# Optimization experiments

Hardware: AMD Instinct MI355X
Metric: run time of the kernel (lower is better)

## Reference

```python
import jax, jax.numpy as jnp
import numpy as np

B, T, C, H = 2, 2048, 1024, 16
D = C // H  # head_dim = 64

def setup_inputs() -> dict:
    key = jax.random.key(0)
    ks = jax.random.split(key, 5)
    x = jax.random.normal(ks[0], (B, T, C), dtype=jnp.float32)
    Wqkv = jax.random.normal(ks[1], (C, 3 * C), dtype=jnp.float32) * 0.02
    bqkv = jnp.zeros((3 * C,), dtype=jnp.float32)
    Wout = jax.random.normal(ks[2], (C, C), dtype=jnp.float32) * 0.02
    bout = jnp.zeros((C,), dtype=jnp.float32)
    return {"x": x, "Wqkv": Wqkv, "bqkv": bqkv, "Wout": Wout, "bout": bout}

def reference(x, Wqkv, bqkv, Wout, bout):
    Bb, Tt, Cc = x.shape
    qkv = x @ Wqkv + bqkv                       # [B,T,3C]
    qkv = qkv.reshape(Bb, Tt, 3, H, D)
    qkv = jnp.transpose(qkv, (2, 0, 3, 1, 4))   # [3,B,H,T,D]
    q, k, v = qkv[0], qkv[1], qkv[2]
    scale = 1.0 / np.sqrt(D).astype(np.float32)
    scores = jnp.einsum('bhqd,bhkd->bhqk', q, k) * scale  # [B,H,T,T]
    causal = jnp.tril(jnp.ones((Tt, Tt), dtype=bool))
    scores = jnp.where(causal[None, None, :, :], scores, jnp.float32(-jnp.inf))
    attn = jax.nn.softmax(scores, axis=-1)
    out = jnp.einsum('bhqk,bhkd->bhqd', attn, v)          # [B,H,T,D]
    out = jnp.transpose(out, (0, 2, 1, 3)).reshape(Bb, Tt, Cc)
    return out @ Wout + bout
```

## Files before the change

### kernel.cpp

```cpp
#include <hip/hip_runtime.h>

#define Bc 2
#define Tc 2048
#define Cc 1024
#define Hc 16
#define Dc 64
#define Mtot (Bc*Tc)
#define Kdim Cc
#define N1 (3*Cc)
#define N2 Cc

typedef __attribute__((ext_vector_type(8))) short short8;
typedef __attribute__((ext_vector_type(4))) float float4v;

__device__ __forceinline__ unsigned short f2bf(float f) {
  unsigned int u = __builtin_bit_cast(unsigned int, f);
  u += 0x7FFFu + ((u >> 16) & 1u);
  return (unsigned short)(u >> 16);
}

__device__ __forceinline__ unsigned int pk_bf16(float a, float b) {
#if __has_builtin(__builtin_amdgcn_cvt_pk_bf16_f32)
  typedef __attribute__((ext_vector_type(2))) __bf16 bf16x2;
  bf16x2 v = __builtin_amdgcn_cvt_pk_bf16_f32(a, b);
  return __builtin_bit_cast(unsigned int, v);
#else
  return (unsigned int)f2bf(a) | ((unsigned int)f2bf(b) << 16);
#endif
}

__device__ __forceinline__ void gl2lds16(const unsigned short* g, unsigned short* l) {
  __builtin_amdgcn_global_load_lds((const __attribute__((address_space(1))) void*)g,
                                   (__attribute__((address_space(3))) void*)l, 16, 0, 0);
}

__global__ __launch_bounds__(256) void k_prep(const float* __restrict__ wqkv,
                                              const float* __restrict__ wout,
                                              const float* __restrict__ x,
                                              unsigned short* __restrict__ wqkvT,
                                              unsigned short* __restrict__ woutT,
                                              unsigned short* __restrict__ xb) {
  const int bx = blockIdx.x;
  if (bx >= 128) {
    int idx = ((bx - 128) * 32 + blockIdx.y) * 256 + threadIdx.x;
    float4 v = ((const float4*)x)[idx];
    uint2 o;
    o.x = pk_bf16(v.x, v.y);
    o.y = pk_bf16(v.z, v.w);
    ((uint2*)xb)[idx] = o;
    return;
  }
  __shared__ float tile[32][33];
  const float* w;  unsigned short* wT;  int N, n0;
  if (bx < 96) { w = wqkv; wT = wqkvT; N = N1; n0 = bx * 32; }
  else         { w = wout; wT = woutT; N = N2; n0 = (bx - 96) * 32; }
  const int k0 = blockIdx.y * 32;
  int tx = threadIdx.x & 31, ty = threadIdx.x >> 5;
  for (int i = 0; i < 4; ++i)
    tile[ty + 8*i][tx] = w[(size_t)(k0 + ty + 8*i) * N + n0 + tx];
  __syncthreads();
  for (int i = 0; i < 4; ++i)
    wT[(size_t)(n0 + ty + 8*i) * Kdim + k0 + tx] = f2bf(tile[tx][ty + 8*i]);
}

__global__ __launch_bounds__(256) void k_gemm_qkv(const unsigned short* __restrict__ A,
                                                  const unsigned short* __restrict__ BT,
                                                  const float* __restrict__ bias,
                                                  unsigned short* __restrict__ qkv) {
  __shared__ alignas(16) unsigned short smem[64*136 + 64];
  unsigned short* As = smem;
  unsigned short* Bs = smem + 4096;
  const int m0 = blockIdx.y * 128, n0 = blockIdx.x * 128;
  const int tid = threadIdx.x;
  const int w = tid >> 6, lane = tid & 63;
  const int ln = lane & 15, qd = lane >> 4;
  const int wm = w >> 1, wn = w & 1;
  const int c0 = tid, c1 = tid + 256;
  const int row0 = c0 >> 2, ko0 = (c0 & 3) * 8;
  const int row1 = c1 >> 2, ko1 = (c1 & 3) * 8;
  const float4v zero4 = {0.f, 0.f, 0.f, 0.f};
  float4v acc[4][4];
  for (int i = 0; i < 4; ++i) for (int j = 0; j < 4; ++j) acc[i][j] = zero4;
  for (int kk = 0; kk < Kdim; kk += 32) {
    __syncthreads();
    gl2lds16(A  + (size_t)(m0 + row0) * Kdim + kk + ko0, As + c0 * 8);
    gl2lds16(A  + (size_t)(m0 + row1) * Kdim + kk + ko1, As + c1 * 8);
    gl2lds16(BT + (size_t)(n0 + row0) * Kdim + kk + ko0, Bs + c0 * 8);
    gl2lds16(BT + (size_t)(n0 + row1) * Kdim + kk + ko1, Bs + c1 * 8);
    __syncthreads();
    short8 af[4], bf[4];
    for (int i = 0; i < 4; ++i)
      af[i] = *(const short8*)(As + (wm*64 + i*16 + ln) * 32 + qd*8);
    for (int j = 0; j < 4; ++j)
      bf[j] = *(const short8*)(Bs + (wn*64 + j*16 + ln) * 32 + qd*8);
    for (int i = 0; i < 4; ++i)
      for (int j = 0; j < 4; ++j)
        acc[i][j] = __builtin_amdgcn_mfma_f32_16x16x32_bf16(af[i], bf[j], acc[i][j], 0, 0, 0);
  }
  const int s = n0 >> 10;
  if (s < 2) {
    const float scale = (s == 0) ? 0.125f : 1.0f;
    for (int i = 0; i < 4; ++i) {
      int mbase = m0 + wm*64 + i*16 + qd*4;
      for (int j = 0; j < 4; ++j) {
        int ncol = n0 + wn*64 + j*16 + ln;
        float bv = bias[ncol];
        int rem = ncol & 1023;
        int h = rem >> 6, d = rem & 63;
        for (int r = 0; r < 4; ++r) {
          int m = mbase + r;
          int b = m >> 11, t = m & 2047;
          float val = (acc[i][j][r] + bv) * scale;
          qkv[((((size_t)s*Bc + b)*Hc + h)*Tc + t)*Dc + d] = f2bf(val);
        }
      }
    }
  } else {
    unsigned short* vbase = qkv + (size_t)2*Bc*Hc*Tc*Dc;
    const int b = m0 >> 11, t0 = m0 & 2047;
    const int h0 = (n0 & 1023) >> 6;
    for (int p = 0; p < 2; ++p) {
      __syncthreads();
      if (wn == p) {
        for (int i = 0; i < 4; ++i) {
          int tl = wm*64 + i*16 + qd*4;
          for (int j = 0; j < 4; ++j) {
            int dl = j*16 + ln;
            float bv = bias[n0 + p*64 + dl];
            uint2 pk;
            pk.x = pk_bf16(acc[i][j][0] + bv, acc[i][j][1] + bv);
            pk.y = pk_bf16(acc[i][j][2] + bv, acc[i][j][3] + bv);
            *(uint2*)(smem + dl*136 + tl) = pk;
          }
        }
      }
      __syncthreads();
      for (int ii = 0; ii < 4; ++ii) {
        int idx = tid + 256*ii;
        int row = idx >> 4, c16 = idx & 15;
        int4 v = *(const int4*)(smem + row*136 + c16*8);
        *(int4*)(vbase + (((size_t)b*Hc + h0 + p)*Dc + row)*Tc + t0 + c16*8) = v;
      }
    }
  }
}

__global__ __launch_bounds__(256) void k_gemm_out(const unsigned short* __restrict__ A,
                                                  const unsigned short* __restrict__ BT,
                                                  const float* __restrict__ bias,
                                                  float* __restrict__ out) {
  __shared__ alignas(16) unsigned short As[64*32];
  __shared__ alignas(16) unsigned short Bs[128*32];
  const int m0 = blockIdx.y * 64, n0 = blockIdx.x * 128;
  const int tid = threadIdx.x;
  const int w = tid >> 6, lane = tid & 63;
  const int ln = lane & 15, qd = lane >> 4;
  const int wm = w >> 1, wn = w & 1;
  const int arow = tid >> 2, ako = (tid & 3) * 8;
  const int c0 = tid, c1 = tid + 256;
  const int brow0 = c0 >> 2, bko0 = (c0 & 3) * 8;
  const int brow1 = c1 >> 2, bko1 = (c1 & 3) * 8;
  const float4v zero4 = {0.f, 0.f, 0.f, 0.f};
  float4v acc[2][4];
  for (int i = 0; i < 2; ++i) for (int j = 0; j < 4; ++j) acc[i][j] = zero4;
  for (int kk = 0; kk < Kdim; kk += 32) {
    __syncthreads();
    gl2lds16(A  + (size_t)(m0 + arow)  * Kdim + kk + ako,  As + tid * 8);
    gl2lds16(BT + (size_t)(n0 + brow0) * Kdim + kk + bko0, Bs + c0 * 8);
    gl2lds16(BT + (size_t)(n0 + brow1) * Kdim + kk + bko1, Bs + c1 * 8);
    __syncthreads();
    short8 af[2], bf[4];
    for (int i = 0; i < 2; ++i)
      af[i] = *(const short8*)(As + (wm*32 + i*16 + ln) * 32 + qd*8);
    for (int j = 0; j < 4; ++j)
      bf[j] = *(const short8*)(Bs + (wn*64 + j*16 + ln) * 32 + qd*8);
    for (int i = 0; i < 2; ++i)
      for (int j = 0; j < 4; ++j)
        acc[i][j] = __builtin_amdgcn_mfma_f32_16x16x32_bf16(af[i], bf[j], acc[i][j], 0, 0, 0);
  }
  for (int i = 0; i < 2; ++i) {
    int mbase = m0 + wm*32 + i*16 + qd*4;
    for (int j = 0; j < 4; ++j) {
      int ncol = n0 + wn*64 + j*16 + ln;
      float bv = bias[ncol];
      for (int r = 0; r < 4; ++r)
        out[(size_t)(mbase + r) * N2 + ncol] = acc[i][j][r] + bv;
    }
  }
}

__device__ __forceinline__ void attn_substep(
    const unsigned short* __restrict__ Ks, const unsigned short* __restrict__ Vt,
    unsigned short* __restrict__ pw,
    const short8 qa0, const short8 qa1,
    float4v* o, float& m_i, float& l_i,
    int k0, int myq, bool mask, int ln, int qd)
{
  const float L2E = 1.44269504f;
  const float4v zero4 = {0.f, 0.f, 0.f, 0.f};
  float4v s[4];
  for (int ki = 0; ki < 4; ++ki) {
    s[ki] = zero4;
    const unsigned short* kr = Ks + (ki*16 + ln)*72;
    short8 kf0 = *(const short8*)(kr + qd*8);
    short8 kf1 = *(const short8*)(kr + 32 + qd*8);
    s[ki] = __builtin_amdgcn_mfma_f32_16x16x32_bf16(kf0, qa0, s[ki], 0, 0, 0);
    s[ki] = __builtin_amdgcn_mfma_f32_16x16x32_bf16(kf1, qa1, s[ki], 0, 0, 0);
  }
  if (mask) {
    for (int ki = 0; ki < 4; ++ki) {
      int key = k0 + ki*16 + qd*4;
      for (int r = 0; r < 4; ++r)
        if (key + r > myq) s[ki][r] = -1e30f;
    }
  }
  float mt = -1e30f;
  for (int ki = 0; ki < 4; ++ki)
    for (int r = 0; r < 4; ++r) mt = fmaxf(mt, s[ki][r]);
  mt = fmaxf(mt, __shfl_xor(mt, 16));
  mt = fmaxf(mt, __shfl_xor(mt, 32));
  float mn = fmaxf(m_i, mt);
  float al = exp2f((m_i - mn) * L2E);
  m_i = mn;
  float st = 0.f;
  for (int ki = 0; ki < 4; ++ki)
    for (int r = 0; r < 4; ++r) {
      s[ki][r] = exp2f((s[ki][r] - mn) * L2E);
      st += s[ki][r];
    }
  st += __shfl_xor(st, 16);
  st += __shfl_xor(st, 32);
  l_i = l_i * al + st;
  for (int dt = 0; dt < 4; ++dt)
    for (int r = 0; r < 4; ++r) o[dt][r] *= al;
  for (int ki = 0; ki < 4; ++ki) {
    uint2 p2;
    p2.x = pk_bf16(s[ki][0], s[ki][1]);
    p2.y = pk_bf16(s[ki][2], s[ki][3]);
    *(uint2*)(pw + ln*72 + ki*16 + qd*4) = p2;
  }
  short8 pb0 = *(const short8*)(pw + ln*72 + qd*8);
  short8 pb1 = *(const short8*)(pw + ln*72 + 32 + qd*8);
  for (int dt = 0; dt < 4; ++dt) {
    const unsigned short* vr = Vt + (dt*16 + ln)*72;
    short8 va0 = *(const short8*)(vr + qd*8);
    short8 va1 = *(const short8*)(vr + 32 + qd*8);
    o[dt] = __builtin_amdgcn_mfma_f32_16x16x32_bf16(va0, pb0, o[dt], 0, 0, 0);
    o[dt] = __builtin_amdgcn_mfma_f32_16x16x32_bf16(va1, pb1, o[dt], 0, 0, 0);
  }
}

__global__ __launch_bounds__(256) void k_attn(const unsigned short* __restrict__ qb,
                                              const unsigned short* __restrict__ kb,
                                              const unsigned short* __restrict__ vT,
                                              unsigned short* __restrict__ ob) {
  __shared__ alignas(16) unsigned short Ks[2][64*72];
  __shared__ alignas(16) unsigned short Vt[2][64*72];
  __shared__ alignas(16) unsigned short Ps[4][16*72];
  const int bh = blockIdx.x;
  const int pp = blockIdx.y;
  const int qtA = 31 - pp, qtB = pp;
  const int tid = threadIdx.x;
  const int w = tid >> 6, lane = tid & 63;
  const int ln = lane & 15, qd = lane >> 4;
  const size_t base = (size_t)bh * Tc * Dc;
  const int b = bh >> 4, h = bh & 15;
  const int srow = tid >> 3, scol = (tid & 7) * 8;
  const float4v zero4 = {0.f, 0.f, 0.f, 0.f};
  unsigned short* pw = Ps[w];

  const int myqA = qtA*64 + w*16 + ln;
  const int myqB = qtB*64 + w*16 + ln;
  const unsigned short* qrA = qb + base + (size_t)myqA * Dc;
  const unsigned short* qrB = qb + base + (size_t)myqB * Dc;
  short8 qaA0 = *(const short8*)(qrA + qd*8);
  short8 qaA1 = *(const short8*)(qrA + 32 + qd*8);
  short8 qaB0 = *(const short8*)(qrB + qd*8);
  short8 qaB1 = *(const short8*)(qrB + 32 + qd*8);
  float4v oA[4], oB[4];
  for (int dt = 0; dt < 4; ++dt) { oA[dt] = zero4; oB[dt] = zero4; }
  float mA = -1e30f, lA = 0.f, mB = -1e30f, lB = 0.f;

  {
    int4 k0v = *(const int4*)(kb + base + (size_t)srow * Dc + scol);
    int4 k1v = *(const int4*)(kb + base + (size_t)(srow + 32) * Dc + scol);
    int4 v0v = *(const int4*)(vT + base + (size_t)srow * Tc + scol);
    int4 v1v = *(const int4*)(vT + base + (size_t)(srow + 32) * Tc + scol);
    *(int4*)(Ks[0] + srow*72 + scol)      = k0v;
    *(int4*)(Ks[0] + (srow+32)*72 + scol) = k1v;
    *(int4*)(Vt[0] + srow*72 + scol)      = v0v;
    *(int4*)(Vt[0] + (srow+32)*72 + scol) = v1v;
  }
  __syncthreads();

  for (int kt = 0; kt <= qtA; ++kt) {
    const int cur = kt & 1;
    int4 rk0, rk1, rv0, rv1;
    if (kt < qtA) {
      const int k0n = (kt + 1) * 64;
      rk0 = *(const int4*)(kb + base + (size_t)(k0n + srow) * Dc + scol);
      rk1 = *(const int4*)(kb + base + (size_t)(k0n + srow + 32) * Dc + scol);
      rv0 = *(const int4*)(vT + base + (size_t)srow * Tc + k0n + scol);
      rv1 = *(const int4*)(vT + base + (size_t)(srow + 32) * Tc + k0n + scol);
    }
    attn_substep(Ks[cur], Vt[cur], pw, qaA0, qaA1, oA, mA, lA, kt*64, myqA, kt == qtA, ln, qd);
    if (kt <= qtB)
      attn_substep(Ks[cur], Vt[cur], pw, qaB0, qaB1, oB, mB, lB, kt*64, myqB, kt == qtB, ln, qd);
    if (kt < qtA) {
      const int nxt = cur ^ 1;
      *(int4*)(Ks[nxt] + srow*72 + scol)      = rk0;
      *(int4*)(Ks[nxt] + (srow+32)*72 + scol) = rk1;
      *(int4*)(Vt[nxt] + srow*72 + scol)      = rv0;
      *(int4*)(Vt[nxt] + (srow+32)*72 + scol) = rv1;
      __syncthreads();
    }
  }
  float invA = 1.0f / lA, invB = 1.0f / lB;
  for (int dt = 0; dt < 4; ++dt) {
    uint2 ovA, ovB;
    ovA.x = pk_bf16(oA[dt][0] * invA, oA[dt][1] * invA);
    ovA.y = pk_bf16(oA[dt][2] * invA, oA[dt][3] * invA);
    *(uint2*)(ob + (size_t)(b*Tc + myqA)*Cc + h*Dc + dt*16 + qd*4) = ovA;
    ovB.x = pk_bf16(oB[dt][0] * invB, oB[dt][1] * invB);
    ovB.y = pk_bf16(oB[dt][2] * invB, oB[dt][3] * invB);
    *(uint2*)(ob + (size_t)(b*Tc + myqB)*Cc + h*Dc + dt*16 + qd*4) = ovB;
  }
}

extern "C" void kernel_launch(void* const* d_in, const int* in_sizes, int n_in,
                              void* d_out, int out_size, void* d_ws, size_t ws_size,
                              hipStream_t stream) {
  const float* x    = (const float*)d_in[0];
  const float* Wqkv = (const float*)d_in[1];
  const float* bqkv = (const float*)d_in[2];
  const float* Wout = (const float*)d_in[3];
  const float* bout = (const float*)d_in[4];
  float* out = (float*)d_out;

  char* ws = (char*)d_ws;
  unsigned short* xb    = (unsigned short*)ws;
  unsigned short* wqkvT = (unsigned short*)(ws + 8388608);
  unsigned short* woutT = (unsigned short*)(ws + 14680064);
  unsigned short* qkvb  = (unsigned short*)(ws + 16777216);

  k_prep<<<dim3(256, 32), 256, 0, stream>>>(Wqkv, Wout, x, wqkvT, woutT, xb);
  k_gemm_qkv<<<dim3(N1/128, Mtot/128), 256, 0, stream>>>(xb, wqkvT, bqkv, qkvb);
  k_attn<<<dim3(32, 16), 256, 0, stream>>>(qkvb, qkvb + (size_t)Bc*Hc*Tc*Dc,
                                           qkvb + (size_t)2*Bc*Hc*Tc*Dc, xb);
  k_gemm_out<<<dim3(N2/128, Mtot/64), 256, 0, stream>>>(xb, woutT, bout, out);
}
```

Measured before the change: 204.6 us.

## Widen attention key tile to 128 with single-buffered LDS and register prefetch

Doubles the key/value tile processed per iteration from 64 to 128 keys, so each online-softmax update (max/sum reductions, rescale) covers more keys. It replaces the double-buffered shared-memory K/V with a single buffer fed from register-prefetched global loads. The goal is to amortise softmax bookkeeping and barriers over more MFMA work. In exchange, register pressure rises and some fully masked keys are computed on the diagonal tile.

```diff
diff --git a/kernel.cpp b/kernel.cpp
--- a/kernel.cpp
+++ b/kernel.cpp
@@ -189,7 +189,7 @@
   }
 }
 
-__device__ __forceinline__ void attn_substep(
+__device__ __forceinline__ void attn_substep128(
     const unsigned short* __restrict__ Ks, const unsigned short* __restrict__ Vt,
     unsigned short* __restrict__ pw,
     const short8 qa0, const short8 qa1,
@@ -198,8 +198,8 @@
 {
   const float L2E = 1.44269504f;
   const float4v zero4 = {0.f, 0.f, 0.f, 0.f};
-  float4v s[4];
-  for (int ki = 0; ki < 4; ++ki) {
+  float4v s[8];
+  for (int ki = 0; ki < 8; ++ki) {
     s[ki] = zero4;
     const unsigned short* kr = Ks + (ki*16 + ln)*72;
     short8 kf0 = *(const short8*)(kr + qd*8);
@@ -208,14 +208,14 @@
     s[ki] = __builtin_amdgcn_mfma_f32_16x16x32_bf16(kf1, qa1, s[ki], 0, 0, 0);
   }
   if (mask) {
-    for (int ki = 0; ki < 4; ++ki) {
+    for (int ki = 0; ki < 8; ++ki) {
       int key = k0 + ki*16 + qd*4;
       for (int r = 0; r < 4; ++r)
         if (key + r > myq) s[ki][r] = -1e30f;
     }
   }
   float mt = -1e30f;
-  for (int ki = 0; ki < 4; ++ki)
+  for (int ki = 0; ki < 8; ++ki)
     for (int r = 0; r < 4; ++r) mt = fmaxf(mt, s[ki][r]);
   mt = fmaxf(mt, __shfl_xor(mt, 16));
   mt = fmaxf(mt, __shfl_xor(mt, 32));
@@ -223,7 +223,7 @@
   float al = exp2f((m_i - mn) * L2E);
   m_i = mn;
   float st = 0.f;
-  for (int ki = 0; ki < 4; ++ki)
+  for (int ki = 0; ki < 8; ++ki)
     for (int r = 0; r < 4; ++r) {
       s[ki][r] = exp2f((s[ki][r] - mn) * L2E);
       st += s[ki][r];
@@ -233,20 +233,21 @@
   l_i = l_i * al + st;
   for (int dt = 0; dt < 4; ++dt)
     for (int r = 0; r < 4; ++r) o[dt][r] *= al;
-  for (int ki = 0; ki < 4; ++ki) {
+  for (int ki = 0; ki < 8; ++ki) {
     uint2 p2;
     p2.x = pk_bf16(s[ki][0], s[ki][1]);
     p2.y = pk_bf16(s[ki][2], s[ki][3]);
-    *(uint2*)(pw + ln*72 + ki*16 + qd*4) = p2;
-  }
-  short8 pb0 = *(const short8*)(pw + ln*72 + qd*8);
-  short8 pb1 = *(const short8*)(pw + ln*72 + 32 + qd*8);
+    *(uint2*)(pw + ln*136 + ki*16 + qd*4) = p2;
+  }
+  short8 pb[4];
+  for (int c = 0; c < 4; ++c)
+    pb[c] = *(const short8*)(pw + ln*136 + c*32 + qd*8);
   for (int dt = 0; dt < 4; ++dt) {
-    const unsigned short* vr = Vt + (dt*16 + ln)*72;
-    short8 va0 = *(const short8*)(vr + qd*8);
-    short8 va1 = *(const short8*)(vr + 32 + qd*8);
-    o[dt] = __builtin_amdgcn_mfma_f32_16x16x32_bf16(va0, pb0, o[dt], 0, 0, 0);
-    o[dt] = __builtin_amdgcn_mfma_f32_16x16x32_bf16(va1, pb1, o[dt], 0, 0, 0);
+    const unsigned short* vr = Vt + (dt*16 + ln)*136;
+    for (int c = 0; c < 4; ++c) {
+      short8 va = *(const short8*)(vr + c*32 + qd*8);
+      o[dt] = __builtin_amdgcn_mfma_f32_16x16x32_bf16(va, pb[c], o[dt], 0, 0, 0);
+    }
   }
 }
 
@@ -254,20 +255,27 @@
                                               const unsigned short* __restrict__ kb,
                                               const unsigned short* __restrict__ vT,
                                               unsigned short* __restrict__ ob) {
-  __shared__ alignas(16) unsigned short Ks[2][64*72];
-  __shared__ alignas(16) unsigned short Vt[2][64*72];
-  __shared__ alignas(16) unsigned short Ps[4][16*72];
+  __shared__ alignas(16) unsigned short Ks[128*72];
+  __shared__ alignas(16) unsigned short Vt[64*136];
+  __shared__ alignas(16) unsigned short Ps[4][16*136];
   const int bh = blockIdx.x;
   const int pp = blockIdx.y;
   const int qtA = 31 - pp, qtB = pp;
+  const int nktA = (qtA >> 1) + 1, nktB = (qtB >> 1) + 1;
   const int tid = threadIdx.x;
   const int w = tid >> 6, lane = tid & 63;
   const int ln = lane & 15, qd = lane >> 4;
   const size_t base = (size_t)bh * Tc * Dc;
   const int b = bh >> 4, h = bh & 15;
-  const int srow = tid >> 3, scol = (tid & 7) * 8;
   const float4v zero4 = {0.f, 0.f, 0.f, 0.f};
   unsigned short* pw = Ps[w];
+
+  int krow[4], kcol[4], vdr[4], vcl[4];
+  for (int p = 0; p < 4; ++p) {
+    int idx = tid + 256*p;
+    krow[p] = idx >> 3;  kcol[p] = (idx & 7) * 8;
+    vdr[p]  = idx >> 4;  vcl[p]  = (idx & 15) * 8;
+  }
 
   const int myqA = qtA*64 + w*16 + ln;
   const int myqB = qtB*64 + w*16 + ln;
@@ -281,39 +289,29 @@
   for (int dt = 0; dt < 4; ++dt) { oA[dt] = zero4; oB[dt] = zero4; }
   float mA = -1e30f, lA = 0.f, mB = -1e30f, lB = 0.f;
 
-  {
-    int4 k0v = *(const int4*)(kb + base + (size_t)srow * Dc + scol);
-    int4 k1v = *(const int4*)(kb + base + (size_t)(srow + 32) * Dc + scol);
-    int4 v0v = *(const int4*)(vT + base + (size_t)srow * Tc + scol);
-    int4 v1v = *(const int4*)(vT + base + (size_t)(srow + 32) * Tc + scol);
-    *(int4*)(Ks[0] + srow*72 + scol)      = k0v;
-    *(int4*)(Ks[0] + (srow+32)*72 + scol) = k1v;
-    *(int4*)(Vt[0] + srow*72 + scol)      = v0v;
-    *(int4*)(Vt[0] + (srow+32)*72 + scol) = v1v;
-  }
-  __syncthreads();
-
-  for (int kt = 0; kt <= qtA; ++kt) {
-    const int cur = kt & 1;
-    int4 rk0, rk1, rv0, rv1;
-    if (kt < qtA) {
-      const int k0n = (kt + 1) * 64;
-      rk0 = *(const int4*)(kb + base + (size_t)(k0n + srow) * Dc + scol);
-      rk1 = *(const int4*)(kb + base + (size_t)(k0n + srow + 32) * Dc + scol);
-      rv0 = *(const int4*)(vT + base + (size_t)srow * Tc + k0n + scol);
-      rv1 = *(const int4*)(vT + base + (size_t)(srow + 32) * Tc + k0n + scol);
-    }
-    attn_substep(Ks[cur], Vt[cur], pw, qaA0, qaA1, oA, mA, lA, kt*64, myqA, kt == qtA, ln, qd);
-    if (kt <= qtB)
-      attn_substep(Ks[cur], Vt[cur], pw, qaB0, qaB1, oB, mB, lB, kt*64, myqB, kt == qtB, ln, qd);
-    if (kt < qtA) {
-      const int nxt = cur ^ 1;
-      *(int4*)(Ks[nxt] + srow*72 + scol)      = rk0;
-      *(int4*)(Ks[nxt] + (srow+32)*72 + scol) = rk1;
-      *(int4*)(Vt[nxt] + srow*72 + scol)      = rv0;
-      *(int4*)(Vt[nxt] + (srow+32)*72 + scol) = rv1;
-      __syncthreads();
-    }
+  int4 rk[4], rv[4];
+  for (int p = 0; p < 4; ++p) {
+    rk[p] = *(const int4*)(kb + base + (size_t)krow[p] * Dc + kcol[p]);
+    rv[p] = *(const int4*)(vT + base + (size_t)vdr[p] * Tc + vcl[p]);
+  }
+
+  for (int kt = 0; kt < nktA; ++kt) {
+    __syncthreads();
+    for (int p = 0; p < 4; ++p) {
+      *(int4*)(Ks + krow[p]*72 + kcol[p]) = rk[p];
+      *(int4*)(Vt + vdr[p]*136 + vcl[p])  = rv[p];
+    }
+    __syncthreads();
+    if (kt + 1 < nktA) {
+      const int k0n = (kt + 1) * 128;
+      for (int p = 0; p < 4; ++p) {
+        rk[p] = *(const int4*)(kb + base + (size_t)(k0n + krow[p]) * Dc + kcol[p]);
+        rv[p] = *(const int4*)(vT + base + (size_t)vdr[p] * Tc + k0n + vcl[p]);
+      }
+    }
+    attn_substep128(Ks, Vt, pw, qaA0, qaA1, oA, mA, lA, kt*128, myqA, kt == nktA-1, ln, qd);
+    if (kt < nktB)
+      attn_substep128(Ks, Vt, pw, qaB0, qaB1, oB, mB, lB, kt*128, myqB, kt == nktB-1, ln, qd);
   }
   float invA = 1.0f / lA, invB = 1.0f / lB;
   for (int dt = 0; dt < 4; ++dt) {
```

New measurement: 259.7 us. 27.0% more time.
